# Kernel tuning notes

Measured on AMD Instinct MI355X. Metric: run time of the kernel, lower is better.

## Reference

```python
import jax, jax.numpy as jnp
import numpy as np
import math

B, N, M, C, H = 4, 2048, 2048, 512, 4
D_V = C // H          # 128, used for scale and value head dim
D_QK = 2 * C // H     # 256, q/k head dim due to seq-axis split of the 2*dim qkv output
SCALE = D_V ** -0.5
EPS = 1e-12           # F.normalize eps


def _l2norm(t):
    n = jnp.linalg.norm(t, axis=-1, keepdims=True)
    return t / jnp.maximum(n, EPS)


def setup_inputs() -> dict:
    key = jax.random.key(0)
    k1, k2, k3, k4 = jax.random.split(key, 4)
    x = jax.random.normal(k1, (B, N, C), dtype=jnp.float32)
    context = jax.random.normal(k2, (B, M, C), dtype=jnp.float32)
    W_qkv = jax.random.normal(k3, (2 * C, C), dtype=jnp.float32) * 0.02  # torch Linear weight [out,in]
    W_proj = jax.random.normal(k4, (C, C), dtype=jnp.float32) * 0.02
    radius = jnp.ones((H,), dtype=jnp.float32) * math.sqrt(D_V)
    return {"x": x, "context": context, "W_qkv": W_qkv, "W_proj": W_proj, "radius": radius}


def reference(x, context, W_qkv, W_proj, radius):
    # qkv(cat([x, context], dim=1)) then split along sequence: q from x rows, k from context rows
    q = jnp.einsum('bnc,oc->bno', x, W_qkv)        # [B,N,2C]
    k = jnp.einsum('bmc,oc->bmo', context, W_qkv)  # [B,M,2C]
    q = q.reshape(B, N, H, D_QK).transpose(0, 2, 1, 3)       # [B,H,N,256]
    k = k.reshape(B, M, H, D_QK).transpose(0, 2, 1, 3)       # [B,H,M,256]
    v = context.reshape(B, M, H, D_V).transpose(0, 2, 1, 3)  # [B,H,M,128]
    r = radius[None, :, None, None]
    q = _l2norm(q) * r
    k = _l2norm(k) * r
    attn = jnp.einsum('bhnd,bhmd->bhnm', q, k) * SCALE
    attn = jax.nn.softmax(attn, axis=-1)
    out = jnp.einsum('bhnm,bhmd->bhnd', attn, v)
    out = out.transpose(0, 2, 1, 3).reshape(B, N, C)
    return jnp.einsum('bnc,oc->bno', out, W_proj)
```

## Files before the change

kernel.cpp:

```cpp
#include <hip/hip_runtime.h>
#include <hip/hip_bf16.h>
#include <stdint.h>

#define SCALE_F 0.08838834764831845f

typedef __attribute__((ext_vector_type(8))) short short8;
typedef __attribute__((ext_vector_type(4))) float f32x4;
typedef __attribute__((ext_vector_type(16))) float f32x16;

__device__ __forceinline__ void g2l16(const void* g, void* l) {
  __builtin_amdgcn_global_load_lds(
      (const __attribute__((address_space(1))) void*)g,
      (__attribute__((address_space(3))) void*)l, 16, 0, 0);
}

__global__ __launch_bounds__(256) void convert_all(
    const float* __restrict__ x, const float* __restrict__ ctx,
    const float* __restrict__ wqkv, const float* __restrict__ wproj,
    __hip_bfloat16* __restrict__ ab, __hip_bfloat16* __restrict__ wb,
    __hip_bfloat16* __restrict__ wpb)
{
  size_t qi = (size_t)blockIdx.x * 256 + threadIdx.x;
  const float* src; __hip_bfloat16* dst; size_t off;
  if (qi < 1048576)      { src = x;     dst = ab;           off = qi; }
  else if (qi < 2097152) { src = ctx;   dst = ab + 4194304; off = qi - 1048576; }
  else if (qi < 2228224) { src = wqkv;  dst = wb;           off = qi - 2097152; }
  else                   { src = wproj; dst = wpb;          off = qi - 2228224; }
  float4 v = ((const float4*)src)[off];
  union { __hip_bfloat16 h4[4]; uint2 u; } o;
  o.h4[0] = __float2bfloat16(v.x); o.h4[1] = __float2bfloat16(v.y);
  o.h4[2] = __float2bfloat16(v.z); o.h4[3] = __float2bfloat16(v.w);
  ((uint2*)dst)[off] = o.u;
}

__global__ __launch_bounds__(256) void transpose_v(
    const float* __restrict__ ctx, __hip_bfloat16* __restrict__ vt)
{
  __shared__ float tile[128][33];
  const int bid = blockIdx.x;
  const int mt = bid & 63;
  const int bh = bid >> 6;
  const int h = bh & 3, b = bh >> 2;
  const int tid = threadIdx.x;
  for (int i = 0; i < 16; ++i) {
    int idx = i * 256 + tid;
    int mm = idx >> 7, d = idx & 127;
    tile[d][mm] = ctx[((size_t)b * 2048 + mt * 32 + mm) * 512 + h * 128 + d];
  }
  __syncthreads();
  for (int i = 0; i < 16; ++i) {
    int idx = i * 256 + tid;
    int d = idx >> 5, mm = idx & 31;
    vt[((size_t)bh * 128 + d) * 2048 + mt * 32 + mm] = __float2bfloat16(tile[d][mm]);
  }
}

__global__ __launch_bounds__(256) void gemm_nt(
    const __hip_bfloat16* __restrict__ A, const __hip_bfloat16* __restrict__ B,
    float* __restrict__ C, int O, int K, int tiles_o)
{
  __shared__ __hip_bfloat16 sA[128 * 32];
  __shared__ __hip_bfloat16 sB[128 * 32];
  const int tid = threadIdx.x;
  const int wave = tid >> 6, lane = tid & 63;
  const int ln = lane & 15, q = lane >> 4;
  const int br = (blockIdx.x / tiles_o) * 128;
  const int bo = (blockIdx.x % tiles_o) * 128;
  const int wr = (wave >> 1) * 64, wc = (wave & 1) * 64;
  const __hip_bfloat16* Ab = A + (size_t)br * K;
  const __hip_bfloat16* Bb = B + (size_t)bo * K;
  const int row0 = tid >> 2, p0 = tid & 3;
  f32x4 acc[4][4] = {};
  for (int k0 = 0; k0 < K; k0 += 32) {
    for (int i = 0; i < 2; ++i) {
      int row = i * 64 + row0;
      g2l16(Ab + (size_t)row * K + k0 + p0 * 8, (char*)sA + (i * 256 + tid) * 16);
      g2l16(Bb + (size_t)row * K + k0 + p0 * 8, (char*)sB + (i * 256 + tid) * 16);
    }
    __syncthreads();
    short8 af[4], bfr[4];
    for (int mi = 0; mi < 4; ++mi)
      af[mi] = *(const short8*)(sA + (wr + mi * 16 + ln) * 32 + q * 8);
    for (int ni = 0; ni < 4; ++ni)
      bfr[ni] = *(const short8*)(sB + (wc + ni * 16 + ln) * 32 + q * 8);
    for (int mi = 0; mi < 4; ++mi)
      for (int ni = 0; ni < 4; ++ni)
        acc[mi][ni] = __builtin_amdgcn_mfma_f32_16x16x32_bf16(af[mi], bfr[ni], acc[mi][ni], 0, 0, 0);
    __syncthreads();
  }
  for (int mi = 0; mi < 4; ++mi)
    for (int ni = 0; ni < 4; ++ni) {
      int rg = br + wr + mi * 16 + q * 4;
      int cg = bo + wc + ni * 16 + ln;
      for (int r = 0; r < 4; ++r)
        C[(size_t)(rg + r) * O + cg] = acc[mi][ni][r];
    }
}

__global__ __launch_bounds__(256) void normalize_qk(
    const float* __restrict__ proj, const float* __restrict__ radius,
    __hip_bfloat16* __restrict__ qn, __hip_bfloat16* __restrict__ kn)
{
  const int r = blockIdx.x;
  const int h = threadIdx.x >> 6, lane = threadIdx.x & 63;
  float4 v = *(const float4*)(proj + (size_t)r * 1024 + h * 256 + lane * 4);
  float ss = v.x * v.x + v.y * v.y + v.z * v.z + v.w * v.w;
  for (int off = 1; off < 64; off <<= 1) ss += __shfl_xor(ss, off);
  float nrm = fmaxf(sqrtf(ss), 1e-12f);
  const bool isq = r < 8192;
  const int rr = isq ? r : r - 8192;
  const float rad = radius[h];
  const float sc = (isq ? rad * rad * SCALE_F : 1.0f) / nrm;
  __hip_bfloat16* dst = (isq ? qn : kn) +
      ((size_t)((rr >> 11) * 4 + h) * 2048 + (rr & 2047)) * 256 + lane * 4;
  union { __hip_bfloat16 h4[4]; uint2 u; } o;
  o.h4[0] = __float2bfloat16(v.x * sc);
  o.h4[1] = __float2bfloat16(v.y * sc);
  o.h4[2] = __float2bfloat16(v.z * sc);
  o.h4[3] = __float2bfloat16(v.w * sc);
  *(uint2*)dst = o.u;
}

__global__ __launch_bounds__(256, 2) void attn(
    const __hip_bfloat16* __restrict__ qn,
    const __hip_bfloat16* __restrict__ kn,
    const __hip_bfloat16* __restrict__ vt,
    float* __restrict__ Op,
    float* __restrict__ den)
{
  __shared__ __hip_bfloat16 sK[2][32 * 256];
  __shared__ __hip_bfloat16 sV[2][128 * 32];
  __shared__ __hip_bfloat16 sP[4][32 * 40];
  const int tid = threadIdx.x, wave = tid >> 6, lane = tid & 63;
  const int m32 = lane & 31, hi = lane >> 5;
  const int i = blockIdx.x;
  const int bh = (i & 7) + 8 * ((i >> 3) & 1);
  const int half = (i >> 4) & 1;
  const int nt = i >> 5;
  const int mbase = half * 1024;
  const __hip_bfloat16* Q = qn + ((size_t)bh * 2048 + nt * 128 + wave * 32) * 256;
  const __hip_bfloat16* Kp = kn + (size_t)bh * 2048 * 256;
  const __hip_bfloat16* Vp = vt + (size_t)bh * 128 * 2048;

  short8 qf[16];
  for (int kk = 0; kk < 16; ++kk)
    qf[kk] = *(const short8*)(Q + m32 * 256 + kk * 16 + hi * 8);

  f32x16 oacc[4];
  float denom[16];
  for (int v = 0; v < 4; ++v)
    for (int j = 0; j < 16; ++j) oacc[v][j] = 0.f;
  for (int j = 0; j < 16; ++j) denom[j] = 0.f;
  __hip_bfloat16* sPw = sP[wave];

  for (int t = 0; t < 4; ++t) {
    int D = t * 256 + tid, row = D >> 5, cc = D & 31;
    g2l16(Kp + (size_t)(mbase + row) * 256 + ((cc ^ (row & 7)) << 3),
          (char*)sK[0] + D * 16);
  }
  for (int t = 0; t < 2; ++t) {
    int D = t * 256 + tid, rd = D >> 2, cc = D & 3;
    g2l16(Vp + (size_t)rd * 2048 + mbase + ((cc ^ ((rd >> 1) & 3)) << 3),
          (char*)sV[0] + D * 16);
  }
  __syncthreads();

  for (int it = 0; it < 32; ++it) {
    const int cur = it & 1, nxt = cur ^ 1;
    if (it + 1 < 32) {
      const int m1 = mbase + (it + 1) * 32;
      for (int t = 0; t < 4; ++t) {
        int D = t * 256 + tid, row = D >> 5, cc = D & 31;
        g2l16(Kp + (size_t)(m1 + row) * 256 + ((cc ^ (row & 7)) << 3),
              (char*)sK[nxt] + D * 16);
      }
      for (int t = 0; t < 2; ++t) {
        int D = t * 256 + tid, rd = D >> 2, cc = D & 3;
        g2l16(Vp + (size_t)rd * 2048 + m1 + ((cc ^ ((rd >> 1) & 3)) << 3),
              (char*)sV[nxt] + D * 16);
      }
    }
    const __hip_bfloat16* sKc = sK[cur];
    f32x16 sa, sb;
    for (int j = 0; j < 16; ++j) { sa[j] = 0.f; sb[j] = 0.f; }
    for (int kk = 0; kk < 8; ++kk) {
      int ca = kk * 2 + hi, cb = (kk + 8) * 2 + hi;
      short8 kfa = *(const short8*)(sKc + m32 * 256 + ((ca ^ (m32 & 7)) << 3));
      short8 kfb = *(const short8*)(sKc + m32 * 256 + ((cb ^ (m32 & 7)) << 3));
      sa = __builtin_amdgcn_mfma_f32_32x32x16_bf16(qf[kk], kfa, sa, 0, 0, 0);
      sb = __builtin_amdgcn_mfma_f32_32x32x16_bf16(qf[kk + 8], kfb, sb, 0, 0, 0);
    }
    for (int reg = 0; reg < 16; ++reg) {
      float e = __expf(sa[reg] + sb[reg]);
      denom[reg] += e;
      int row = (reg & 3) + 8 * (reg >> 2) + 4 * hi;
      sPw[row * 40 + m32] = __float2bfloat16(e);
    }
    asm volatile("s_waitcnt lgkmcnt(0)" ::: "memory");
    const __hip_bfloat16* sVc = sV[cur];
    for (int kc = 0; kc < 2; ++kc) {
      short8 pf = *(const short8*)(sPw + m32 * 40 + kc * 16 + hi * 8);
      for (int vi = 0; vi < 4; ++vi) {
        int rd = vi * 32 + m32;
        int c = kc * 2 + hi;
        short8 vf = *(const short8*)(sVc + rd * 32 + ((c ^ ((rd >> 1) & 3)) << 3));
        oacc[vi] = __builtin_amdgcn_mfma_f32_32x32x16_bf16(pf, vf, oacc[vi], 0, 0, 0);
      }
    }
    __syncthreads();
  }

  for (int reg = 0; reg < 16; ++reg)
    for (int off = 1; off < 32; off <<= 1)
      denom[reg] += __shfl_xor(denom[reg], off);

  float* Opb = Op + ((size_t)(half * 16 + bh) * 2048) * 128;
  float* denb = den + (size_t)(half * 16 + bh) * 2048;
  const int rbase = nt * 128 + wave * 32;
  for (int vi = 0; vi < 4; ++vi)
    for (int reg = 0; reg < 16; ++reg) {
      int row = rbase + (reg & 3) + 8 * (reg >> 2) + 4 * hi;
      Opb[(size_t)row * 128 + vi * 32 + m32] = oacc[vi][reg];
    }
  if (m32 == 0)
    for (int reg = 0; reg < 16; ++reg)
      denb[rbase + (reg & 3) + 8 * (reg >> 2) + 4 * hi] = denom[reg];
}

__global__ __launch_bounds__(256) void combine(
    const float* __restrict__ Op, const float* __restrict__ den,
    __hip_bfloat16* __restrict__ ob)
{
  int qi = blockIdx.x * 256 + threadIdx.x;
  int r = qi >> 5, dq = qi & 5 * 6 + 1;
  dq = qi & 31;
  int bh = r >> 11, n = r & 2047, b = bh >> 2, h = bh & 3;
  float4 o0 = ((const float4*)Op)[qi];
  float4 o1 = ((const float4*)(Op + 4194304))[qi];
  float inv = 1.0f / (den[r] + den[32768 + r]);
  union { __hip_bfloat16 h4[4]; uint2 u; } o;
  o.h4[0] = __float2bfloat16((o0.x + o1.x) * inv);
  o.h4[1] = __float2bfloat16((o0.y + o1.y) * inv);
  o.h4[2] = __float2bfloat16((o0.z + o1.z) * inv);
  o.h4[3] = __float2bfloat16((o0.w + o1.w) * inv);
  *(uint2*)&ob[((size_t)b * 2048 + n) * 512 + h * 128 + dq * 4] = o.u;
}

extern "C" void kernel_launch(void* const* d_in, const int* in_sizes, int n_in,
                              void* d_out, int out_size, void* d_ws, size_t ws_size,
                              hipStream_t stream) {
  const float* x      = (const float*)d_in[0];
  const float* ctx    = (const float*)d_in[1];
  const float* wqkv   = (const float*)d_in[2];
  const float* wproj  = (const float*)d_in[3];
  const float* radius = (const float*)d_in[4];
  char* ws = (char*)d_ws;
  __hip_bfloat16* ab  = (__hip_bfloat16*)(ws);
  __hip_bfloat16* wb  = (__hip_bfloat16*)(ws + 16777216);
  __hip_bfloat16* wpb = (__hip_bfloat16*)(ws + 17825792);
  float*          proj= (float*)(ws + 18350080);
  float*          Op  = proj;
  float*          den = (float*)(ws + 18350080 + 33554432);
  __hip_bfloat16* qn  = (__hip_bfloat16*)(ws + 85458944);
  __hip_bfloat16* kn  = (__hip_bfloat16*)(ws + 102236160);
  __hip_bfloat16* vt  = (__hip_bfloat16*)(ws + 119013376);
  __hip_bfloat16* ob  = (__hip_bfloat16*)(ws + 127401984);
  float* out = (float*)d_out;

  convert_all<<<8960, 256, 0, stream>>>(x, ctx, wqkv, wproj, ab, wb, wpb);
  transpose_v<<<1024, 256, 0, stream>>>(ctx, vt);
  gemm_nt<<<1024, 256, 0, stream>>>(ab, wb, proj, 1024, 512, 8);
  normalize_qk<<<16384, 256, 0, stream>>>(proj, radius, qn, kn);
  attn<<<512, 256, 0, stream>>>(qn, kn, vt, Op, den);
  combine<<<4096, 256, 0, stream>>>(Op, den, ob);
  gemm_nt<<<256, 256, 0, stream>>>(ob, wpb, out, 512, 512, 4);
}
```

Baseline: 227.2 us.

## Warp-specialize attention into QK/softmax and PV/loader waves; store qkv projection as bf16

```diff
diff --git a/kernel.cpp b/kernel.cpp
--- a/kernel.cpp
+++ b/kernel.cpp
@@ -12,6 +12,10 @@
   __builtin_amdgcn_global_load_lds(
       (const __attribute__((address_space(1))) void*)g,
       (__attribute__((address_space(3))) void*)l, 16, 0, 0);
+}
+
+__device__ __forceinline__ float bf2f(unsigned short s) {
+  union { unsigned int i; float f; } c; c.i = ((unsigned int)s) << 16; return c.f;
 }
 
 __global__ __launch_bounds__(256) void convert_all(
@@ -55,9 +59,10 @@
   }
 }
 
+template <typename OUT>
 __global__ __launch_bounds__(256) void gemm_nt(
     const __hip_bfloat16* __restrict__ A, const __hip_bfloat16* __restrict__ B,
-    float* __restrict__ C, int O, int K, int tiles_o)
+    OUT* __restrict__ C, int O, int K, int tiles_o)
 {
   __shared__ __hip_bfloat16 sA[128 * 32];
   __shared__ __hip_bfloat16 sB[128 * 32];
@@ -92,19 +97,26 @@
     for (int ni = 0; ni < 4; ++ni) {
       int rg = br + wr + mi * 16 + q * 4;
       int cg = bo + wc + ni * 16 + ln;
-      for (int r = 0; r < 4; ++r)
-        C[(size_t)(rg + r) * O + cg] = acc[mi][ni][r];
+      for (int r = 0; r < 4; ++r) {
+        float v = acc[mi][ni][r];
+        if constexpr (sizeof(OUT) == 2)
+          C[(size_t)(rg + r) * O + cg] = __float2bfloat16(v);
+        else
+          C[(size_t)(rg + r) * O + cg] = v;
+      }
     }
 }
 
 __global__ __launch_bounds__(256) void normalize_qk(
-    const float* __restrict__ proj, const float* __restrict__ radius,
+    const __hip_bfloat16* __restrict__ proj, const float* __restrict__ radius,
     __hip_bfloat16* __restrict__ qn, __hip_bfloat16* __restrict__ kn)
 {
   const int r = blockIdx.x;
   const int h = threadIdx.x >> 6, lane = threadIdx.x & 63;
-  float4 v = *(const float4*)(proj + (size_t)r * 1024 + h * 256 + lane * 4);
-  float ss = v.x * v.x + v.y * v.y + v.z * v.z + v.w * v.w;
+  union { uint2 u; unsigned short s[4]; } pu;
+  pu.u = *(const uint2*)(proj + (size_t)r * 1024 + h * 256 + lane * 4);
+  float v0 = bf2f(pu.s[0]), v1 = bf2f(pu.s[1]), v2 = bf2f(pu.s[2]), v3 = bf2f(pu.s[3]);
+  float ss = v0 * v0 + v1 * v1 + v2 * v2 + v3 * v3;
   for (int off = 1; off < 64; off <<= 1) ss += __shfl_xor(ss, off);
   float nrm = fmaxf(sqrtf(ss), 1e-12f);
   const bool isq = r < 8192;
@@ -114,10 +126,10 @@
   __hip_bfloat16* dst = (isq ? qn : kn) +
       ((size_t)((rr >> 11) * 4 + h) * 2048 + (rr & 2047)) * 256 + lane * 4;
   union { __hip_bfloat16 h4[4]; uint2 u; } o;
-  o.h4[0] = __float2bfloat16(v.x * sc);
-  o.h4[1] = __float2bfloat16(v.y * sc);
-  o.h4[2] = __float2bfloat16(v.z * sc);
-  o.h4[3] = __float2bfloat16(v.w * sc);
+  o.h4[0] = __float2bfloat16(v0 * sc);
+  o.h4[1] = __float2bfloat16(v1 * sc);
+  o.h4[2] = __float2bfloat16(v2 * sc);
+  o.h4[3] = __float2bfloat16(v3 * sc);
   *(uint2*)dst = o.u;
 }
 
@@ -130,7 +142,7 @@
 {
   __shared__ __hip_bfloat16 sK[2][32 * 256];
   __shared__ __hip_bfloat16 sV[2][128 * 32];
-  __shared__ __hip_bfloat16 sP[4][32 * 40];
+  __shared__ __hip_bfloat16 sP[128 * 40];
   const int tid = threadIdx.x, wave = tid >> 6, lane = tid & 63;
   const int m32 = lane & 31, hi = lane >> 5;
   const int i = blockIdx.x;
@@ -138,93 +150,116 @@
   const int half = (i >> 4) & 1;
   const int nt = i >> 5;
   const int mbase = half * 1024;
-  const __hip_bfloat16* Q = qn + ((size_t)bh * 2048 + nt * 128 + wave * 32) * 256;
+  const int flip = (i >> 8) & 1;
+  const bool isQK = ((wave >> 1) ^ flip) == 0;
+  const int wsub = wave & 1;
   const __hip_bfloat16* Kp = kn + (size_t)bh * 2048 * 256;
   const __hip_bfloat16* Vp = vt + (size_t)bh * 128 * 2048;
 
-  short8 qf[16];
-  for (int kk = 0; kk < 16; ++kk)
-    qf[kk] = *(const short8*)(Q + m32 * 256 + kk * 16 + hi * 8);
-
-  f32x16 oacc[4];
-  float denom[16];
-  for (int v = 0; v < 4; ++v)
-    for (int j = 0; j < 16; ++j) oacc[v][j] = 0.f;
-  for (int j = 0; j < 16; ++j) denom[j] = 0.f;
-  __hip_bfloat16* sPw = sP[wave];
-
-  for (int t = 0; t < 4; ++t) {
-    int D = t * 256 + tid, row = D >> 5, cc = D & 31;
-    g2l16(Kp + (size_t)(mbase + row) * 256 + ((cc ^ (row & 7)) << 3),
-          (char*)sK[0] + D * 16);
+  if (isQK) {
+    short8 qf[2][16];
+    const __hip_bfloat16* Q = qn + ((size_t)bh * 2048 + nt * 128 + wsub * 64) * 256;
+    for (int sub = 0; sub < 2; ++sub)
+      for (int kk = 0; kk < 16; ++kk)
+        qf[sub][kk] = *(const short8*)(Q + (sub * 32 + m32) * 256 + kk * 16 + hi * 8);
+    float dn0[16], dn1[16];
+    for (int j = 0; j < 16; ++j) { dn0[j] = 0.f; dn1[j] = 0.f; }
+    __syncthreads();
+    for (int it = 0; it < 32; ++it) {
+      const __hip_bfloat16* sKc = sK[it & 1];
+      f32x16 s0, s1;
+      for (int j = 0; j < 16; ++j) { s0[j] = 0.f; s1[j] = 0.f; }
+      for (int kk = 0; kk < 16; ++kk) {
+        int c = kk * 2 + hi;
+        short8 kf = *(const short8*)(sKc + m32 * 256 + ((c ^ (m32 & 7)) << 3));
+        s0 = __builtin_amdgcn_mfma_f32_32x32x16_bf16(qf[0][kk], kf, s0, 0, 0, 0);
+        s1 = __builtin_amdgcn_mfma_f32_32x32x16_bf16(qf[1][kk], kf, s1, 0, 0, 0);
+      }
+      for (int reg = 0; reg < 16; ++reg) {
+        int r0 = wsub * 64 + (reg & 3) + 8 * (reg >> 2) + 4 * hi;
+        float e0 = __expf(s0[reg]), e1 = __expf(s1[reg]);
+        dn0[reg] += e0; dn1[reg] += e1;
+        sP[r0 * 40 + m32] = __float2bfloat16(e0);
+        sP[(r0 + 32) * 40 + m32] = __float2bfloat16(e1);
+      }
+      __syncthreads();
+      __syncthreads();
+    }
+    for (int reg = 0; reg < 16; ++reg)
+      for (int off = 1; off < 32; off <<= 1) {
+        dn0[reg] += __shfl_xor(dn0[reg], off);
+        dn1[reg] += __shfl_xor(dn1[reg], off);
+      }
+    if (m32 == 0) {
+      float* denb = den + (size_t)(half * 16 + bh) * 2048 + nt * 128;
+      for (int reg = 0; reg < 16; ++reg) {
+        int r0 = wsub * 64 + (reg & 3) + 8 * (reg >> 2) + 4 * hi;
+        denb[r0] = dn0[reg];
+        denb[r0 + 32] = dn1[reg];
+      }
+    }
+  } else {
+    f32x16 oacc[4][2];
+    for (int a = 0; a < 4; ++a)
+      for (int b2 = 0; b2 < 2; ++b2)
+        for (int j = 0; j < 16; ++j) oacc[a][b2][j] = 0.f;
+    for (int j = 0; j < 8; ++j) {
+      int D = j * 128 + wsub * 64 + lane;
+      int row = D >> 5, cc = D & 31;
+      g2l16(Kp + (size_t)(mbase + row) * 256 + ((cc ^ (row & 7)) << 3),
+            (char*)sK[0] + D * 16);
+    }
+    for (int j = 0; j < 4; ++j) {
+      int D = j * 128 + wsub * 64 + lane;
+      int rd = D >> 2, cc = D & 3;
+      g2l16(Vp + (size_t)rd * 2048 + mbase + ((cc ^ ((rd >> 1) & 3)) << 3),
+            (char*)sV[0] + D * 16);
+    }
+    __syncthreads();
+    for (int it = 0; it < 32; ++it) {
+      const int cur = it & 1, nxt = cur ^ 1;
+      if (it + 1 < 32) {
+        const int m1 = mbase + (it + 1) * 32;
+        for (int j = 0; j < 8; ++j) {
+          int D = j * 128 + wsub * 64 + lane;
+          int row = D >> 5, cc = D & 31;
+          g2l16(Kp + (size_t)(m1 + row) * 256 + ((cc ^ (row & 7)) << 3),
+                (char*)sK[nxt] + D * 16);
+        }
+        for (int j = 0; j < 4; ++j) {
+          int D = j * 128 + wsub * 64 + lane;
+          int rd = D >> 2, cc = D & 3;
+          g2l16(Vp + (size_t)rd * 2048 + m1 + ((cc ^ ((rd >> 1) & 3)) << 3),
+                (char*)sV[nxt] + D * 16);
+        }
+      }
+      __syncthreads();
+      const __hip_bfloat16* sVc = sV[cur];
+      for (int kc = 0; kc < 2; ++kc) {
+        short8 vf0, vf1;
+        {
+          int rd0 = wsub * 64 + m32, rd1 = wsub * 64 + 32 + m32;
+          int c = kc * 2 + hi;
+          vf0 = *(const short8*)(sVc + rd0 * 32 + ((c ^ ((rd0 >> 1) & 3)) << 3));
+          vf1 = *(const short8*)(sVc + rd1 * 32 + ((c ^ ((rd1 >> 1) & 3)) << 3));
+        }
+        for (int ms = 0; ms < 4; ++ms) {
+          short8 pf = *(const short8*)(sP + (ms * 32 + m32) * 40 + kc * 16 + hi * 8);
+          oacc[ms][0] = __builtin_amdgcn_mfma_f32_32x32x16_bf16(pf, vf0, oacc[ms][0], 0, 0, 0);
+          oacc[ms][1] = __builtin_amdgcn_mfma_f32_32x32x16_bf16(pf, vf1, oacc[ms][1], 0, 0, 0);
+        }
+      }
+      __syncthreads();
+    }
+    float* Opb = Op + ((size_t)(half * 16 + bh) * 2048 + nt * 128) * 128;
+    for (int ms = 0; ms < 4; ++ms)
+      for (int ns = 0; ns < 2; ++ns)
+        for (int reg = 0; reg < 16; ++reg) {
+          int row = ms * 32 + (reg & 3) + 8 * (reg >> 2) + 4 * hi;
+          int col = wsub * 64 + ns * 32 + m32;
+          Opb[(size_t)row * 128 + col] = oacc[ms][ns][reg];
+        }
   }
-  for (int t = 0; t < 2; ++t) {
-    int D = t * 256 + tid, rd = D >> 2, cc = D & 3;
-    g2l16(Vp + (size_t)rd * 2048 + mbase + ((cc ^ ((rd >> 1) & 3)) << 3),
-          (char*)sV[0] + D * 16);
-  }
-  __syncthreads();
-
-  for (int it = 0; it < 32; ++it) {
-    const int cur = it & 1, nxt = cur ^ 1;
-    if (it + 1 < 32) {
-      const int m1 = mbase + (it + 1) * 32;
-      for (int t = 0; t < 4; ++t) {
-        int D = t * 256 + tid, row = D >> 5, cc = D & 31;
-        g2l16(Kp + (size_t)(m1 + row) * 256 + ((cc ^ (row & 7)) << 3),
-              (char*)sK[nxt] + D * 16);
-      }
-      for (int t = 0; t < 2; ++t) {
-        int D = t * 256 + tid, rd = D >> 2, cc = D & 3;
-        g2l16(Vp + (size_t)rd * 2048 + m1 + ((cc ^ ((rd >> 1) & 3)) << 3),
-              (char*)sV[nxt] + D * 16);
-      }
-    }
-    const __hip_bfloat16* sKc = sK[cur];
-    f32x16 sa, sb;
-    for (int j = 0; j < 16; ++j) { sa[j] = 0.f; sb[j] = 0.f; }
-    for (int kk = 0; kk < 8; ++kk) {
-      int ca = kk * 2 + hi, cb = (kk + 8) * 2 + hi;
-      short8 kfa = *(const short8*)(sKc + m32 * 256 + ((ca ^ (m32 & 7)) << 3));
-      short8 kfb = *(const short8*)(sKc + m32 * 256 + ((cb ^ (m32 & 7)) << 3));
-      sa = __builtin_amdgcn_mfma_f32_32x32x16_bf16(qf[kk], kfa, sa, 0, 0, 0);
-      sb = __builtin_amdgcn_mfma_f32_32x32x16_bf16(qf[kk + 8], kfb, sb, 0, 0, 0);
-    }
-    for (int reg = 0; reg < 16; ++reg) {
-      float e = __expf(sa[reg] + sb[reg]);
-      denom[reg] += e;
-      int row = (reg & 3) + 8 * (reg >> 2) + 4 * hi;
-      sPw[row * 40 + m32] = __float2bfloat16(e);
-    }
-    asm volatile("s_waitcnt lgkmcnt(0)" ::: "memory");
-    const __hip_bfloat16* sVc = sV[cur];
-    for (int kc = 0; kc < 2; ++kc) {
-      short8 pf = *(const short8*)(sPw + m32 * 40 + kc * 16 + hi * 8);
-      for (int vi = 0; vi < 4; ++vi) {
-        int rd = vi * 32 + m32;
-        int c = kc * 2 + hi;
-        short8 vf = *(const short8*)(sVc + rd * 32 + ((c ^ ((rd >> 1) & 3)) << 3));
-        oacc[vi] = __builtin_amdgcn_mfma_f32_32x32x16_bf16(pf, vf, oacc[vi], 0, 0, 0);
-      }
-    }
-    __syncthreads();
-  }
-
-  for (int reg = 0; reg < 16; ++reg)
-    for (int off = 1; off < 32; off <<= 1)
-      denom[reg] += __shfl_xor(denom[reg], off);
-
-  float* Opb = Op + ((size_t)(half * 16 + bh) * 2048) * 128;
-  float* denb = den + (size_t)(half * 16 + bh) * 2048;
-  const int rbase = nt * 128 + wave * 32;
-  for (int vi = 0; vi < 4; ++vi)
-    for (int reg = 0; reg < 16; ++reg) {
-      int row = rbase + (reg & 3) + 8 * (reg >> 2) + 4 * hi;
-      Opb[(size_t)row * 128 + vi * 32 + m32] = oacc[vi][reg];
-    }
-  if (m32 == 0)
-    for (int reg = 0; reg < 16; ++reg)
-      denb[rbase + (reg & 3) + 8 * (reg >> 2) + 4 * hi] = denom[reg];
 }
 
 __global__ __launch_bounds__(256) void combine(
@@ -232,8 +267,7 @@
     __hip_bfloat16* __restrict__ ob)
 {
   int qi = blockIdx.x * 256 + threadIdx.x;
-  int r = qi >> 5, dq = qi & 5 * 6 + 1;
-  dq = qi & 31;
+  int r = qi >> 5, dq = qi & 31;
   int bh = r >> 11, n = r & 2047, b = bh >> 2, h = bh & 3;
   float4 o0 = ((const float4*)Op)[qi];
   float4 o1 = ((const float4*)(Op + 4194304))[qi];
@@ -258,8 +292,8 @@
   __hip_bfloat16* ab  = (__hip_bfloat16*)(ws);
   __hip_bfloat16* wb  = (__hip_bfloat16*)(ws + 16777216);
   __hip_bfloat16* wpb = (__hip_bfloat16*)(ws + 17825792);
-  float*          proj= (float*)(ws + 18350080);
-  float*          Op  = proj;
+  __hip_bfloat16* proj= (__hip_bfloat16*)(ws + 18350080);
+  float*          Op  = (float*)(ws + 18350080);
   float*          den = (float*)(ws + 18350080 + 33554432);
   __hip_bfloat16* qn  = (__hip_bfloat16*)(ws + 85458944);
   __hip_bfloat16* kn  = (__hip_bfloat16*)(ws + 102236160);
@@ -269,9 +303,9 @@
 
   convert_all<<<8960, 256, 0, stream>>>(x, ctx, wqkv, wproj, ab, wb, wpb);
   transpose_v<<<1024, 256, 0, stream>>>(ctx, vt);
-  gemm_nt<<<1024, 256, 0, stream>>>(ab, wb, proj, 1024, 512, 8);
+  gemm_nt<__hip_bfloat16><<<1024, 256, 0, stream>>>(ab, wb, proj, 1024, 512, 8);
   normalize_qk<<<16384, 256, 0, stream>>>(proj, radius, qn, kn);
   attn<<<512, 256, 0, stream>>>(qn, kn, vt, Op, den);
   combine<<<4096, 256, 0, stream>>>(Op, den, ob);
-  gemm_nt<<<256, 256, 0, stream>>>(ob, wpb, out, 512, 512, 4);
-}
+  gemm_nt<float><<<256, 256, 0, stream>>>(ob, wpb, out, 512, 512, 4);
+}
```

Measured after the change: 228.6 us. About the same (+0.6%).

## Software-pipeline QK scores in attention and shrink intermediate traffic

Applied to the files above, without the earlier changes.

```diff
diff --git a/kernel.cpp b/kernel.cpp
--- a/kernel.cpp
+++ b/kernel.cpp
@@ -14,18 +14,20 @@
       (__attribute__((address_space(3))) void*)l, 16, 0, 0);
 }
 
-__global__ __launch_bounds__(256) void convert_all(
-    const float* __restrict__ x, const float* __restrict__ ctx,
-    const float* __restrict__ wqkv, const float* __restrict__ wproj,
-    __hip_bfloat16* __restrict__ ab, __hip_bfloat16* __restrict__ wb,
-    __hip_bfloat16* __restrict__ wpb)
+__device__ __forceinline__ float bf2f(unsigned short s) {
+  union { unsigned int i; float f; } c; c.i = ((unsigned int)s) << 16; return c.f;
+}
+
+__global__ __launch_bounds__(256) void convert_xw(
+    const float* __restrict__ x, const float* __restrict__ wqkv,
+    const float* __restrict__ wproj, __hip_bfloat16* __restrict__ ab,
+    __hip_bfloat16* __restrict__ wb, __hip_bfloat16* __restrict__ wpb)
 {
   size_t qi = (size_t)blockIdx.x * 256 + threadIdx.x;
   const float* src; __hip_bfloat16* dst; size_t off;
-  if (qi < 1048576)      { src = x;     dst = ab;           off = qi; }
-  else if (qi < 2097152) { src = ctx;   dst = ab + 4194304; off = qi - 1048576; }
-  else if (qi < 2228224) { src = wqkv;  dst = wb;           off = qi - 2097152; }
-  else                   { src = wproj; dst = wpb;          off = qi - 2228224; }
+  if (qi < 1048576)      { src = x;     dst = ab;  off = qi; }
+  else if (qi < 1179648) { src = wqkv;  dst = wb;  off = qi - 1048576; }
+  else                   { src = wproj; dst = wpb; off = qi - 1179648; }
   float4 v = ((const float4*)src)[off];
   union { __hip_bfloat16 h4[4]; uint2 u; } o;
   o.h4[0] = __float2bfloat16(v.x); o.h4[1] = __float2bfloat16(v.y);
@@ -33,8 +35,9 @@
   ((uint2*)dst)[off] = o.u;
 }
 
-__global__ __launch_bounds__(256) void transpose_v(
-    const float* __restrict__ ctx, __hip_bfloat16* __restrict__ vt)
+__global__ __launch_bounds__(256) void ctx_pack(
+    const float* __restrict__ ctx, __hip_bfloat16* __restrict__ vt,
+    __hip_bfloat16* __restrict__ ab)
 {
   __shared__ float tile[128][33];
   const int bid = blockIdx.x;
@@ -45,7 +48,10 @@
   for (int i = 0; i < 16; ++i) {
     int idx = i * 256 + tid;
     int mm = idx >> 7, d = idx & 127;
-    tile[d][mm] = ctx[((size_t)b * 2048 + mt * 32 + mm) * 512 + h * 128 + d];
+    size_t gidx = ((size_t)b * 2048 + mt * 32 + mm) * 512 + h * 128 + d;
+    float v = ctx[gidx];
+    tile[d][mm] = v;
+    ab[4194304 + gidx] = __float2bfloat16(v);
   }
   __syncthreads();
   for (int i = 0; i < 16; ++i) {
@@ -55,9 +61,10 @@
   }
 }
 
+template <typename OUT>
 __global__ __launch_bounds__(256) void gemm_nt(
     const __hip_bfloat16* __restrict__ A, const __hip_bfloat16* __restrict__ B,
-    float* __restrict__ C, int O, int K, int tiles_o)
+    OUT* __restrict__ C, int O, int K, int tiles_o)
 {
   __shared__ __hip_bfloat16 sA[128 * 32];
   __shared__ __hip_bfloat16 sB[128 * 32];
@@ -92,19 +99,26 @@
     for (int ni = 0; ni < 4; ++ni) {
       int rg = br + wr + mi * 16 + q * 4;
       int cg = bo + wc + ni * 16 + ln;
-      for (int r = 0; r < 4; ++r)
-        C[(size_t)(rg + r) * O + cg] = acc[mi][ni][r];
+      for (int r = 0; r < 4; ++r) {
+        float v = acc[mi][ni][r];
+        if constexpr (sizeof(OUT) == 2)
+          C[(size_t)(rg + r) * O + cg] = __float2bfloat16(v);
+        else
+          C[(size_t)(rg + r) * O + cg] = v;
+      }
     }
 }
 
 __global__ __launch_bounds__(256) void normalize_qk(
-    const float* __restrict__ proj, const float* __restrict__ radius,
+    const __hip_bfloat16* __restrict__ proj, const float* __restrict__ radius,
     __hip_bfloat16* __restrict__ qn, __hip_bfloat16* __restrict__ kn)
 {
   const int r = blockIdx.x;
   const int h = threadIdx.x >> 6, lane = threadIdx.x & 63;
-  float4 v = *(const float4*)(proj + (size_t)r * 1024 + h * 256 + lane * 4);
-  float ss = v.x * v.x + v.y * v.y + v.z * v.z + v.w * v.w;
+  union { uint2 u; unsigned short s[4]; } pu;
+  pu.u = *(const uint2*)(proj + (size_t)r * 1024 + h * 256 + lane * 4);
+  float v0 = bf2f(pu.s[0]), v1 = bf2f(pu.s[1]), v2 = bf2f(pu.s[2]), v3 = bf2f(pu.s[3]);
+  float ss = v0 * v0 + v1 * v1 + v2 * v2 + v3 * v3;
   for (int off = 1; off < 64; off <<= 1) ss += __shfl_xor(ss, off);
   float nrm = fmaxf(sqrtf(ss), 1e-12f);
   const bool isq = r < 8192;
@@ -114,10 +128,10 @@
   __hip_bfloat16* dst = (isq ? qn : kn) +
       ((size_t)((rr >> 11) * 4 + h) * 2048 + (rr & 2047)) * 256 + lane * 4;
   union { __hip_bfloat16 h4[4]; uint2 u; } o;
-  o.h4[0] = __float2bfloat16(v.x * sc);
-  o.h4[1] = __float2bfloat16(v.y * sc);
-  o.h4[2] = __float2bfloat16(v.z * sc);
-  o.h4[3] = __float2bfloat16(v.w * sc);
+  o.h4[0] = __float2bfloat16(v0 * sc);
+  o.h4[1] = __float2bfloat16(v1 * sc);
+  o.h4[2] = __float2bfloat16(v2 * sc);
+  o.h4[3] = __float2bfloat16(v3 * sc);
   *(uint2*)dst = o.u;
 }
 
@@ -128,7 +142,7 @@
     float* __restrict__ Op,
     float* __restrict__ den)
 {
-  __shared__ __hip_bfloat16 sK[2][32 * 256];
+  __shared__ __hip_bfloat16 sK[3][32 * 256];
   __shared__ __hip_bfloat16 sV[2][128 * 32];
   __shared__ __hip_bfloat16 sP[4][32 * 40];
   const int tid = threadIdx.x, wave = tid >> 6, lane = tid & 63;
@@ -138,13 +152,15 @@
   const int half = (i >> 4) & 1;
   const int nt = i >> 5;
   const int mbase = half * 1024;
-  const __hip_bfloat16* Q = qn + ((size_t)bh * 2048 + nt * 128 + wave * 32) * 256;
   const __hip_bfloat16* Kp = kn + (size_t)bh * 2048 * 256;
   const __hip_bfloat16* Vp = vt + (size_t)bh * 128 * 2048;
 
   short8 qf[16];
-  for (int kk = 0; kk < 16; ++kk)
-    qf[kk] = *(const short8*)(Q + m32 * 256 + kk * 16 + hi * 8);
+  {
+    const __hip_bfloat16* Q = qn + ((size_t)bh * 2048 + nt * 128 + wave * 32) * 256;
+    for (int kk = 0; kk < 16; ++kk)
+      qf[kk] = *(const short8*)(Q + m32 * 256 + kk * 16 + hi * 8);
+  }
 
   f32x16 oacc[4];
   float denom[16];
@@ -153,51 +169,56 @@
   for (int j = 0; j < 16; ++j) denom[j] = 0.f;
   __hip_bfloat16* sPw = sP[wave];
 
-  for (int t = 0; t < 4; ++t) {
-    int D = t * 256 + tid, row = D >> 5, cc = D & 31;
-    g2l16(Kp + (size_t)(mbase + row) * 256 + ((cc ^ (row & 7)) << 3),
-          (char*)sK[0] + D * 16);
-  }
-  for (int t = 0; t < 2; ++t) {
-    int D = t * 256 + tid, rd = D >> 2, cc = D & 3;
-    g2l16(Vp + (size_t)rd * 2048 + mbase + ((cc ^ ((rd >> 1) & 3)) << 3),
-          (char*)sV[0] + D * 16);
-  }
+#define STAGE_K(tile, buf)                                                   \
+  for (int t = 0; t < 4; ++t) {                                              \
+    int D = t * 256 + tid, row = D >> 5, cc = D & 31;                        \
+    g2l16(Kp + (size_t)(mbase + (tile) * 32 + row) * 256 + ((cc ^ (row & 7)) << 3), \
+          (char*)sK[buf] + D * 16);                                          \
+  }
+#define STAGE_V(tile, buf)                                                   \
+  for (int t = 0; t < 2; ++t) {                                              \
+    int D = t * 256 + tid, rd = D >> 2, cc = D & 3;                          \
+    g2l16(Vp + (size_t)rd * 2048 + mbase + (tile) * 32 + ((cc ^ ((rd >> 1) & 3)) << 3), \
+          (char*)sV[buf] + D * 16);                                          \
+  }
+
+  STAGE_K(0, 0);
+  STAGE_V(0, 0);
   __syncthreads();
+  STAGE_K(1, 1);
+  f32x16 S_cur;
+  for (int j = 0; j < 16; ++j) S_cur[j] = 0.f;
+  {
+    const __hip_bfloat16* sKc = sK[0];
+    for (int kk = 0; kk < 16; ++kk) {
+      int c = kk * 2 + hi;
+      short8 kf = *(const short8*)(sKc + m32 * 256 + ((c ^ (m32 & 7)) << 3));
+      S_cur = __builtin_amdgcn_mfma_f32_32x32x16_bf16(qf[kk], kf, S_cur, 0, 0, 0);
+    }
+  }
+  __syncthreads();
 
   for (int it = 0; it < 32; ++it) {
-    const int cur = it & 1, nxt = cur ^ 1;
+    if (it + 2 < 32) { STAGE_K(it + 2, (it + 2) % 3); }
+    if (it + 1 < 32) { STAGE_V(it + 1, (it + 1) & 1); }
+    f32x16 S_next;
+    for (int j = 0; j < 16; ++j) S_next[j] = 0.f;
     if (it + 1 < 32) {
-      const int m1 = mbase + (it + 1) * 32;
-      for (int t = 0; t < 4; ++t) {
-        int D = t * 256 + tid, row = D >> 5, cc = D & 31;
-        g2l16(Kp + (size_t)(m1 + row) * 256 + ((cc ^ (row & 7)) << 3),
-              (char*)sK[nxt] + D * 16);
+      const __hip_bfloat16* sKc = sK[(it + 1) % 3];
+      for (int kk = 0; kk < 16; ++kk) {
+        int c = kk * 2 + hi;
+        short8 kf = *(const short8*)(sKc + m32 * 256 + ((c ^ (m32 & 7)) << 3));
+        S_next = __builtin_amdgcn_mfma_f32_32x32x16_bf16(qf[kk], kf, S_next, 0, 0, 0);
       }
-      for (int t = 0; t < 2; ++t) {
-        int D = t * 256 + tid, rd = D >> 2, cc = D & 3;
-        g2l16(Vp + (size_t)rd * 2048 + m1 + ((cc ^ ((rd >> 1) & 3)) << 3),
-              (char*)sV[nxt] + D * 16);
-      }
-    }
-    const __hip_bfloat16* sKc = sK[cur];
-    f32x16 sa, sb;
-    for (int j = 0; j < 16; ++j) { sa[j] = 0.f; sb[j] = 0.f; }
-    for (int kk = 0; kk < 8; ++kk) {
-      int ca = kk * 2 + hi, cb = (kk + 8) * 2 + hi;
-      short8 kfa = *(const short8*)(sKc + m32 * 256 + ((ca ^ (m32 & 7)) << 3));
-      short8 kfb = *(const short8*)(sKc + m32 * 256 + ((cb ^ (m32 & 7)) << 3));
-      sa = __builtin_amdgcn_mfma_f32_32x32x16_bf16(qf[kk], kfa, sa, 0, 0, 0);
-      sb = __builtin_amdgcn_mfma_f32_32x32x16_bf16(qf[kk + 8], kfb, sb, 0, 0, 0);
     }
     for (int reg = 0; reg < 16; ++reg) {
-      float e = __expf(sa[reg] + sb[reg]);
+      float e = __expf(S_cur[reg]);
       denom[reg] += e;
       int row = (reg & 3) + 8 * (reg >> 2) + 4 * hi;
       sPw[row * 40 + m32] = __float2bfloat16(e);
     }
     asm volatile("s_waitcnt lgkmcnt(0)" ::: "memory");
-    const __hip_bfloat16* sVc = sV[cur];
+    const __hip_bfloat16* sVc = sV[it & 1];
     for (int kc = 0; kc < 2; ++kc) {
       short8 pf = *(const short8*)(sPw + m32 * 40 + kc * 16 + hi * 8);
       for (int vi = 0; vi < 4; ++vi) {
@@ -208,23 +229,25 @@
       }
     }
     __syncthreads();
-  }
+    S_cur = S_next;
+  }
+#undef STAGE_K
+#undef STAGE_V
 
   for (int reg = 0; reg < 16; ++reg)
     for (int off = 1; off < 32; off <<= 1)
       denom[reg] += __shfl_xor(denom[reg], off);
 
-  float* Opb = Op + ((size_t)(half * 16 + bh) * 2048) * 128;
-  float* denb = den + (size_t)(half * 16 + bh) * 2048;
-  const int rbase = nt * 128 + wave * 32;
+  float* Opb = Op + ((size_t)(half * 16 + bh) * 2048 + nt * 128 + wave * 32) * 128;
+  float* denb = den + (size_t)(half * 16 + bh) * 2048 + nt * 128 + wave * 32;
   for (int vi = 0; vi < 4; ++vi)
     for (int reg = 0; reg < 16; ++reg) {
-      int row = rbase + (reg & 3) + 8 * (reg >> 2) + 4 * hi;
+      int row = (reg & 3) + 8 * (reg >> 2) + 4 * hi;
       Opb[(size_t)row * 128 + vi * 32 + m32] = oacc[vi][reg];
     }
   if (m32 == 0)
     for (int reg = 0; reg < 16; ++reg)
-      denb[rbase + (reg & 3) + 8 * (reg >> 2) + 4 * hi] = denom[reg];
+      denb[(reg & 3) + 8 * (reg >> 2) + 4 * hi] = denom[reg];
 }
 
 __global__ __launch_bounds__(256) void combine(
@@ -232,8 +255,7 @@
     __hip_bfloat16* __restrict__ ob)
 {
   int qi = blockIdx.x * 256 + threadIdx.x;
-  int r = qi >> 5, dq = qi & 5 * 6 + 1;
-  dq = qi & 31;
+  int r = qi >> 5, dq = qi & 31;
   int bh = r >> 11, n = r & 2047, b = bh >> 2, h = bh & 3;
   float4 o0 = ((const float4*)Op)[qi];
   float4 o1 = ((const float4*)(Op + 4194304))[qi];
@@ -258,20 +280,20 @@
   __hip_bfloat16* ab  = (__hip_bfloat16*)(ws);
   __hip_bfloat16* wb  = (__hip_bfloat16*)(ws + 16777216);
   __hip_bfloat16* wpb = (__hip_bfloat16*)(ws + 17825792);
-  float*          proj= (float*)(ws + 18350080);
-  float*          Op  = proj;
-  float*          den = (float*)(ws + 18350080 + 33554432);
+  __hip_bfloat16* proj= (__hip_bfloat16*)(ws + 18350080);
+  float*          Op  = (float*)(ws + 18350080);
+  float*          den = (float*)(ws + 51904512);
   __hip_bfloat16* qn  = (__hip_bfloat16*)(ws + 85458944);
   __hip_bfloat16* kn  = (__hip_bfloat16*)(ws + 102236160);
   __hip_bfloat16* vt  = (__hip_bfloat16*)(ws + 119013376);
   __hip_bfloat16* ob  = (__hip_bfloat16*)(ws + 127401984);
   float* out = (float*)d_out;
 
-  convert_all<<<8960, 256, 0, stream>>>(x, ctx, wqkv, wproj, ab, wb, wpb);
-  transpose_v<<<1024, 256, 0, stream>>>(ctx, vt);
-  gemm_nt<<<1024, 256, 0, stream>>>(ab, wb, proj, 1024, 512, 8);
+  convert_xw<<<4864, 256, 0, stream>>>(x, wqkv, wproj, ab, wb, wpb);
+  ctx_pack<<<1024, 256, 0, stream>>>(ctx, vt, ab);
+  gemm_nt<__hip_bfloat16><<<1024, 256, 0, stream>>>(ab, wb, proj, 1024, 512, 8);
   normalize_qk<<<16384, 256, 0, stream>>>(proj, radius, qn, kn);
   attn<<<512, 256, 0, stream>>>(qn, kn, vt, Op, den);
   combine<<<4096, 256, 0, stream>>>(Op, den, ob);
-  gemm_nt<<<256, 256, 0, stream>>>(ob, wpb, out, 512, 512, 4);
-}
+  gemm_nt<float><<<256, 256, 0, stream>>>(ob, wpb, out, 512, 512, 4);
+}
```

Measured after the change: 227.5 us. About the same (+0.2%).
